# Performance work log

Hardware: AMD Instinct MI355X
Metric: run time of the kernel (lower is better)

Reference implementation:

```python
import jax, jax.numpy as jnp
import numpy as np

FORGET_BIAS = 1.0

def _lstm_layer(x_seq, W, b):
    # x_seq: [T, B, D]; W: [D+H, 4H]; b: [4H]
    T, B, _ = x_seq.shape
    H = W.shape[1] // 4
    def step(carry, x):
        c, h = carry
        z = jnp.concatenate([x, h], axis=1) @ W + b  # [B, 4H]
        i, j, f, o = jnp.split(z, 4, axis=1)          # BasicLSTMCell gate order
        new_c = c * jax.nn.sigmoid(f + FORGET_BIAS) + jax.nn.sigmoid(i) * jnp.tanh(j)
        new_h = jnp.tanh(new_c) * jax.nn.sigmoid(o)
        return (new_c, new_h), new_h
    init = (jnp.zeros((B, H), x_seq.dtype), jnp.zeros((B, H), x_seq.dtype))
    _, out = jax.lax.scan(step, init, x_seq)
    return out  # [T, B, H]

def setup_inputs() -> dict:
    key = jax.random.key(0)
    k0, k1, k2 = jax.random.split(key, 3)
    T, B, D, H = 256, 64, 1024, 1024
    scale = 0.05  # keep gates out of saturation
    return {
        "input_seq": jax.random.normal(k0, (T, B, D), dtype=jnp.float32),
        "W0": jax.random.normal(k1, (D + H, 4 * H), dtype=jnp.float32) * scale,
        "b0": jnp.zeros((4 * H,), dtype=jnp.float32),
        "W1": jax.random.normal(k2, (H + H, 4 * H), dtype=jnp.float32) * scale,
        "b1": jnp.zeros((4 * H,), dtype=jnp.float32),
    }

def reference(input_seq, W0, b0, W1, b1):
    # 2-layer static LSTM (training=False -> no dropout)
    h1 = _lstm_layer(input_seq, W0, b0)
    h2 = _lstm_layer(h1, W1, b1)
    return h2
```

## Files before the change

### kernel.cpp

```cpp
#include <hip/hip_runtime.h>
#include <cmath>


typedef _Float16 half8 __attribute__((ext_vector_type(8)));
typedef float f32x4 __attribute__((ext_vector_type(4)));

constexpr int Tt = 256, Gg = 4096;
constexpr size_t HPACK = 65536;
constexpr int NBLK = 256;
constexpr unsigned WLDS_BYTES = 131072;
constexpr unsigned ZP_FLOATS = 8 * 16 * 17;
constexpr unsigned HSTAGE_BYTES = 64 * 8 * 2;
constexpr unsigned SMEM_BYTES = WLDS_BYTES + ZP_FLOATS * 4 + HSTAGE_BYTES + 16;

__device__ __forceinline__ float sigmoidf_(float x) { return 1.f / (1.f + expf(-x)); }

__global__ void pack_w_kernel(const float* __restrict__ W0, const float* __restrict__ W1,
                              _Float16* __restrict__ WP0, _Float16* __restrict__ WP1) {
    int idx = blockIdx.x * 256 + threadIdx.x;
    const float* src = blockIdx.y ? W1 : W0;
    _Float16* dst = blockIdx.y ? WP1 : WP0;
    int lane = idx & 63;
    int kt = (idx >> 6) & 63;
    int nt = idx >> 12;
    int p = nt * 16 + (lane & 15);
    int col = (p & 3) * 1024 + (p >> 2);
    int kbase = kt * 32 + (lane >> 4) * 8;
    half8 v;
#pragma unroll
    for (int j = 0; j < 8; ++j) v[j] = (_Float16)src[(size_t)(kbase + j) * Gg + col];
    *reinterpret_cast<half8*>(dst + (size_t)idx * 8) = v;
}

__global__ void pack_bias_kernel(const float* __restrict__ b0, const float* __restrict__ b1,
                                 float* __restrict__ bp0, float* __restrict__ bp1) {
    int idx = blockIdx.x * 256 + threadIdx.x;
    int l = idx >> 12, p = idx & 4095;
    int col = (p & 3) * 1024 + (p >> 2);
    (l ? bp1 : bp0)[p] = (l ? b1 : b0)[col];
}

__global__ void pack_a_kernel(const float* __restrict__ X, _Float16* __restrict__ XP) {
    int idx = blockIdx.x * 256 + threadIdx.x;
    int lane = idx & 63;
    int kt = (idx >> 6) & 31;
    int mt = idx >> 11;
    int m = mt * 16 + (lane & 15);
    int kbase = kt * 32 + (lane >> 4) * 8;
    const float* srow = X + (size_t)m * 1024 + kbase;
    half8 v;
#pragma unroll
    for (int j = 0; j < 8; ++j) v[j] = (_Float16)srow[j];
    *reinterpret_cast<half8*>(XP + (size_t)idx * 8) = v;
}

__device__ __forceinline__ void scout_wait(const unsigned* rep, int* tokLds, int t) {
    if ((threadIdx.x & 63) == 0) {
        unsigned spins = 0;
        while (__hip_atomic_load(rep, __ATOMIC_RELAXED, __HIP_MEMORY_SCOPE_AGENT) < 128u) {
            __builtin_amdgcn_s_sleep(1);
            if (++spins > (1u << 18)) break;
        }
        __hip_atomic_store(tokLds, t, __ATOMIC_RELAXED, __HIP_MEMORY_SCOPE_WORKGROUP);
    }
    asm volatile("" ::: "memory");
}

__device__ __forceinline__ void lds_wait(const int* tokLds, int t) {
    unsigned spins = 0;
    while (__hip_atomic_load(tokLds, __ATOMIC_RELAXED, __HIP_MEMORY_SCOPE_WORKGROUP) < t) {
        __builtin_amdgcn_s_sleep(1);
        if (++spins > (1u << 20)) break;
    }
    asm volatile("" ::: "memory");
}

struct FArgs {
    const _Float16* XP;
    const _Float16* WP0;
    const _Float16* WP1;
    const float* bp0;
    const float* bp1;
    _Float16* h1r;
    _Float16* h2r;
    unsigned* h1f;
    unsigned* h2f;
    float* out;
};

__global__ __launch_bounds__(1024, 4) void lstm_fused(FArgs a) {
    extern __shared__ char smem[];
    _Float16* wlds = (_Float16*)smem;
    float* zp = (float*)(smem + WLDS_BYTES);
    _Float16* hstage = (_Float16*)(smem + WLDS_BYTES + ZP_FLOATS * 4);
    int* tok = (int*)(smem + WLDS_BYTES + ZP_FLOATS * 4 + HSTAGE_BYTES);

    const int tid = threadIdx.x;
    const int layer = blockIdx.x >> 7;
    const int cg = blockIdx.x & 127;
    const int rep = cg & 7;

    const _Float16* wsrc = (layer ? a.WP1 : a.WP0) + (size_t)cg * 65536;
    for (int i = tid; i < 8192; i += 1024)
        ((half8*)wlds)[i] = ((const half8*)wsrc)[i];
    for (int i = tid; i < (int)ZP_FLOATS; i += 1024) zp[i] = 0.f;
    if (tid == 0) { tok[0] = -1; tok[1] = -1; }

    float creg = 0.f;
    float bias4[4] = {0.f, 0.f, 0.f, 0.f};
    if (tid < 512) {
        int hl = tid & 7;
        const float* bp = layer ? a.bp1 : a.bp0;
#pragma unroll
        for (int g = 0; g < 4; ++g) bias4[g] = bp[cg * 32 + hl * 4 + g];
    }
    __syncthreads();

    const int lane = tid & 63, wv = tid >> 6;
    const int mt = wv & 3, kq = wv >> 2;
    const int r0 = (lane >> 4) * 4, ccc = lane & 15;
    const int ktL = (kq & 1) * 16;

    for (int t = 0; t < Tt; ++t) {
        if (layer == 0) {
            if (kq >= 2 && t > 0) {
                if (wv == 8) scout_wait(a.h1f + ((size_t)(t - 1) * 8 + rep) * 32, tok + 0, t);
                else         lds_wait(tok + 0, t);
            }
        } else {
            if (kq < 2) {
                if (wv == 0) scout_wait(a.h1f + ((size_t)t * 8 + rep) * 32, tok + 0, t);
                else         lds_wait(tok + 0, t);
            } else if (t > 0) {
                if (wv == 8) scout_wait(a.h2f + ((size_t)(t - 1) * 8 + rep) * 32, tok + 1, t);
                else         lds_wait(tok + 1, t);
            }
        }

        const _Float16* srcA;
        if (layer == 0)
            srcA = (kq < 2) ? (a.XP + (size_t)t * HPACK) : (a.h1r + (size_t)t * HPACK);
        else
            srcA = (kq < 2) ? (a.h1r + (size_t)(t + 1) * HPACK) : (a.h2r + (size_t)t * HPACK);

        const half8* ap = (const half8*)srcA + ((size_t)mt * 32 + ktL) * 64 + lane;
        const half8* bq0 = (const half8*)wlds + ((size_t)(0 * 64 + kq * 16)) * 64 + lane;
        const half8* bq1 = (const half8*)wlds + ((size_t)(1 * 64 + kq * 16)) * 64 + lane;
        f32x4 ac0 = {0.f, 0.f, 0.f, 0.f}, ac1 = {0.f, 0.f, 0.f, 0.f};
#pragma unroll
        for (int i = 0; i < 16; ++i) {
            half8 av = ap[i * 64];
            ac0 = __builtin_amdgcn_mfma_f32_16x16x32_f16(av, bq0[i * 64], ac0, 0, 0, 0);
            ac1 = __builtin_amdgcn_mfma_f32_16x16x32_f16(av, bq1[i * 64], ac1, 0, 0, 0);
        }
#pragma unroll
        for (int r = 0; r < 4; ++r) {
            atomicAdd(&zp[((mt * 2 + 0) * 16 + r0 + r) * 17 + ccc], ac0[r]);
            atomicAdd(&zp[((mt * 2 + 1) * 16 + r0 + r) * 17 + ccc], ac1[r]);
        }
        __syncthreads();

        if (tid < 512) {
            int b = tid >> 3, hl = tid & 7;
            float z[4];
#pragma unroll
            for (int g = 0; g < 4; ++g) {
                int c = hl * 4 + g;
                z[g] = zp[(((b >> 4) * 2 + (c >> 4)) * 16 + (b & 15)) * 17 + (c & 15)] + bias4[g];
            }
            float cn = creg * sigmoidf_(z[2] + 1.0f) + sigmoidf_(z[0]) * tanhf(z[1]);
            float hn = tanhf(cn) * sigmoidf_(z[3]);
            creg = cn;
            hstage[b * 8 + hl] = (_Float16)hn;
            if (layer) a.out[(size_t)t * 65536 + (size_t)b * 1024 + (cg * 8 + hl)] = hn;
        }
        __syncthreads();

        if (tid < 256) {
            int b = tid >> 2, pr = tid & 3;
            unsigned lo = (unsigned)__builtin_bit_cast(unsigned short, hstage[b * 8 + 2 * pr]);
            unsigned hi = (unsigned)__builtin_bit_cast(unsigned short, hstage[b * 8 + 2 * pr + 1]);
            unsigned val = lo | (hi << 16);
            _Float16* hdst = (layer ? a.h2r : a.h1r) + (size_t)(t + 1) * HPACK;
            size_t dw = (((size_t)(b >> 4) * 32 + (cg >> 2)) * 64 + (size_t)(cg & 3) * 16 + (b & 15)) * 4 + pr;
            __hip_atomic_store((unsigned*)hdst + dw, val, __ATOMIC_RELAXED, __HIP_MEMORY_SCOPE_AGENT);
        }
        for (int i = tid; i < (int)ZP_FLOATS; i += 1024) zp[i] = 0.f;
        __syncthreads();

        if (tid < 8) {
            unsigned* f = (layer ? a.h2f : a.h1f) + ((size_t)t * 8 + tid) * 32;
            (void)__hip_atomic_fetch_add(f, 1u, __ATOMIC_RELAXED, __HIP_MEMORY_SCOPE_AGENT);
        }
    }
}

extern "C" void kernel_launch(void* const* d_in, const int* in_sizes, int n_in,
                              void* d_out, int out_size, void* d_ws, size_t ws_size,
                              hipStream_t stream) {
    const float* X  = (const float*)d_in[0];
    const float* W0 = (const float*)d_in[1];
    const float* b0 = (const float*)d_in[2];
    const float* W1 = (const float*)d_in[3];
    const float* b1 = (const float*)d_in[4];
    float* out = (float*)d_out;

    char* ws = (char*)d_ws;
    size_t off = 0;
    auto take = [&](size_t n) -> void* {
        void* r = ws + off;
        off += (n + 255) & ~(size_t)255;
        return r;
    };

    const size_t WPB = (size_t)2048 * Gg * 2;
    _Float16* WP0 = (_Float16*)take(WPB);
    _Float16* WP1 = (_Float16*)take(WPB);
    float* bp0 = (float*)take(Gg * 4);
    float* bp1 = (float*)take(Gg * 4);
    const size_t APB = (size_t)Tt * 64 * 1024 * 2;
    _Float16* XP = (_Float16*)take(APB);
    const size_t RINGB = (size_t)(Tt + 1) * HPACK * 2;
    _Float16* h1r = (_Float16*)take(RINGB);
    _Float16* h2r = (_Float16*)take(RINGB);
    const size_t FLAGB = (size_t)Tt * 8 * 32 * 4;
    unsigned* h1f = (unsigned*)take(FLAGB);
    unsigned* h2f = (unsigned*)take(FLAGB);

    hipMemsetAsync(h1r, 0, HPACK * 2, stream);
    hipMemsetAsync(h2r, 0, HPACK * 2, stream);
    hipMemsetAsync(h1f, 0, FLAGB, stream);
    hipMemsetAsync(h2f, 0, FLAGB, stream);

    pack_w_kernel<<<dim3(4096, 2), 256, 0, stream>>>(W0, W1, WP0, WP1);
    pack_bias_kernel<<<32, 256, 0, stream>>>(b0, b1, bp0, bp1);
    pack_a_kernel<<<8192, 256, 0, stream>>>(X, XP);

    hipFuncSetAttribute((const void*)lstm_fused,
                        hipFuncAttributeMaxDynamicSharedMemorySize, SMEM_BYTES);

    FArgs fa{XP, WP0, WP1, bp0, bp1, h1r, h2r, h1f, h2f, out};
    void* kp[] = {&fa};
    hipError_t e = hipLaunchCooperativeKernel((const void*)lstm_fused, dim3(NBLK), dim3(1024),
                                              kp, SMEM_BYTES, stream);
    if (e != hipSuccess) {
        lstm_fused<<<dim3(NBLK), dim3(1024), SMEM_BYTES, stream>>>(fa);
    }
    (void)in_sizes; (void)n_in; (void)out_size; (void)ws_size;
}
```

Baseline: 3.979 ms.

## Replace per-step atomic counters with per-wave monotonic flags polled by every wave

```diff
diff --git a/kernel.cpp b/kernel.cpp
--- a/kernel.cpp
+++ b/kernel.cpp
@@ -4,6 +4,7 @@
 
 typedef _Float16 half8 __attribute__((ext_vector_type(8)));
 typedef float f32x4 __attribute__((ext_vector_type(4)));
+typedef unsigned int uint4v __attribute__((ext_vector_type(4)));
 
 constexpr int Tt = 256, Gg = 4096;
 constexpr size_t HPACK = 65536;
@@ -11,7 +12,7 @@
 constexpr unsigned WLDS_BYTES = 131072;
 constexpr unsigned ZP_FLOATS = 8 * 16 * 17;
 constexpr unsigned HSTAGE_BYTES = 64 * 8 * 2;
-constexpr unsigned SMEM_BYTES = WLDS_BYTES + ZP_FLOATS * 4 + HSTAGE_BYTES + 16;
+constexpr unsigned SMEM_BYTES = WLDS_BYTES + ZP_FLOATS * 4 + HSTAGE_BYTES;
 
 __device__ __forceinline__ float sigmoidf_(float x) { return 1.f / (1.f + expf(-x)); }
 
@@ -54,23 +55,22 @@
     *reinterpret_cast<half8*>(XP + (size_t)idx * 8) = v;
 }
 
-__device__ __forceinline__ void scout_wait(const unsigned* rep, int* tokLds, int t) {
-    if ((threadIdx.x & 63) == 0) {
-        unsigned spins = 0;
-        while (__hip_atomic_load(rep, __ATOMIC_RELAXED, __HIP_MEMORY_SCOPE_AGENT) < 128u) {
-            __builtin_amdgcn_s_sleep(1);
-            if (++spins > (1u << 18)) break;
-        }
-        __hip_atomic_store(tokLds, t, __ATOMIC_RELAXED, __HIP_MEMORY_SCOPE_WORKGROUP);
-    }
-    asm volatile("" ::: "memory");
-}
-
-__device__ __forceinline__ void lds_wait(const int* tokLds, int t) {
+__device__ __forceinline__ void wait_flags(const unsigned* flags, unsigned tgt) {
+    int lane = threadIdx.x & 63;
+    const unsigned* p0 = flags + (size_t)lane * 4;
+    const unsigned* p1 = flags + (size_t)(lane + 64) * 4;
     unsigned spins = 0;
-    while (__hip_atomic_load(tokLds, __ATOMIC_RELAXED, __HIP_MEMORY_SCOPE_WORKGROUP) < t) {
+    for (;;) {
+        uint4v f0, f1;
+        asm volatile("global_load_dwordx4 %0, %2, off sc0 sc1\n\t"
+                     "global_load_dwordx4 %1, %3, off sc0 sc1"
+                     : "=v"(f0), "=v"(f1) : "v"(p0), "v"(p1));
+        asm volatile("s_waitcnt vmcnt(0)" ::: "memory");
+        bool ok = f0[0] >= tgt && f0[1] >= tgt && f0[2] >= tgt && f0[3] >= tgt &&
+                  f1[0] >= tgt && f1[1] >= tgt && f1[2] >= tgt && f1[3] >= tgt;
+        if (__all(ok)) break;
         __builtin_amdgcn_s_sleep(1);
-        if (++spins > (1u << 20)) break;
+        if (++spins > (1u << 18)) break;
     }
     asm volatile("" ::: "memory");
 }
@@ -93,18 +93,15 @@
     _Float16* wlds = (_Float16*)smem;
     float* zp = (float*)(smem + WLDS_BYTES);
     _Float16* hstage = (_Float16*)(smem + WLDS_BYTES + ZP_FLOATS * 4);
-    int* tok = (int*)(smem + WLDS_BYTES + ZP_FLOATS * 4 + HSTAGE_BYTES);
 
     const int tid = threadIdx.x;
     const int layer = blockIdx.x >> 7;
     const int cg = blockIdx.x & 127;
-    const int rep = cg & 7;
 
     const _Float16* wsrc = (layer ? a.WP1 : a.WP0) + (size_t)cg * 65536;
     for (int i = tid; i < 8192; i += 1024)
         ((half8*)wlds)[i] = ((const half8*)wsrc)[i];
     for (int i = tid; i < (int)ZP_FLOATS; i += 1024) zp[i] = 0.f;
-    if (tid == 0) { tok[0] = -1; tok[1] = -1; }
 
     float creg = 0.f;
     float bias4[4] = {0.f, 0.f, 0.f, 0.f};
@@ -123,18 +120,10 @@
 
     for (int t = 0; t < Tt; ++t) {
         if (layer == 0) {
-            if (kq >= 2 && t > 0) {
-                if (wv == 8) scout_wait(a.h1f + ((size_t)(t - 1) * 8 + rep) * 32, tok + 0, t);
-                else         lds_wait(tok + 0, t);
-            }
+            if (kq >= 2 && t > 0) wait_flags(a.h1f, (unsigned)t);
         } else {
-            if (kq < 2) {
-                if (wv == 0) scout_wait(a.h1f + ((size_t)t * 8 + rep) * 32, tok + 0, t);
-                else         lds_wait(tok + 0, t);
-            } else if (t > 0) {
-                if (wv == 8) scout_wait(a.h2f + ((size_t)(t - 1) * 8 + rep) * 32, tok + 1, t);
-                else         lds_wait(tok + 1, t);
-            }
+            if (kq < 2)           wait_flags(a.h1f, (unsigned)(t + 1));
+            else if (t > 0)       wait_flags(a.h2f, (unsigned)t);
         }
 
         const _Float16* srcA;
@@ -184,14 +173,15 @@
             _Float16* hdst = (layer ? a.h2r : a.h1r) + (size_t)(t + 1) * HPACK;
             size_t dw = (((size_t)(b >> 4) * 32 + (cg >> 2)) * 64 + (size_t)(cg & 3) * 16 + (b & 15)) * 4 + pr;
             __hip_atomic_store((unsigned*)hdst + dw, val, __ATOMIC_RELAXED, __HIP_MEMORY_SCOPE_AGENT);
+            asm volatile("s_waitcnt vmcnt(0)" ::: "memory");
+            __builtin_amdgcn_sched_barrier(0);
+            if ((tid & 63) == 0) {
+                unsigned* f = (layer ? a.h2f : a.h1f) + (size_t)cg * 4 + wv;
+                __hip_atomic_store(f, (unsigned)(t + 1), __ATOMIC_RELAXED, __HIP_MEMORY_SCOPE_AGENT);
+            }
         }
         for (int i = tid; i < (int)ZP_FLOATS; i += 1024) zp[i] = 0.f;
         __syncthreads();
-
-        if (tid < 8) {
-            unsigned* f = (layer ? a.h2f : a.h1f) + ((size_t)t * 8 + tid) * 32;
-            (void)__hip_atomic_fetch_add(f, 1u, __ATOMIC_RELAXED, __HIP_MEMORY_SCOPE_AGENT);
-        }
     }
 }
 
@@ -223,7 +213,7 @@
     const size_t RINGB = (size_t)(Tt + 1) * HPACK * 2;
     _Float16* h1r = (_Float16*)take(RINGB);
     _Float16* h2r = (_Float16*)take(RINGB);
-    const size_t FLAGB = (size_t)Tt * 8 * 32 * 4;
+    const size_t FLAGB = 128 * 4 * 4;
     unsigned* h1f = (unsigned*)take(FLAGB);
     unsigned* h2f = (unsigned*)take(FLAGB);
 
```

After: 4.399 ms. 1.11x slower.
